# Kernel tuning notes

Measured on AMD Instinct MI355X. Metric: run time of the kernel, lower is better.

## Reference

```python
import jax, jax.numpy as jnp
import numpy as np
from jax import lax

NB = 65536          # voxels (seeds) per batch element
C = 256             # feature dim
NUM_CLASS = 3
MAX_NPOINTS = 4096  # per-batch top-k keep
FPS_NPOINTS = 2048  # farthest-point samples
OFFSET_RANGE = np.array([3.0, 3.0, 2.0], dtype=np.float32)
BN_EPS = 1e-5


def _bn_relu(x, gamma, beta):
    # nn.BatchNorm1d in training mode: batch statistics over N
    m = jnp.mean(x, axis=0)
    v = jnp.var(x, axis=0)
    return jax.nn.relu((x - m) * lax.rsqrt(v + BN_EPS) * gamma + beta)


def _vote_mlp(x, w1, g1, b1, w2, b2):
    # Linear(bias=False) -> BN -> ReLU -> Linear(bias)
    return _bn_relu(x @ w1, g1, b1) @ w2 + b2


def _fps(xyz, k):
    # D-FPS (PointNet++ furthest_point_sample): start at index 0,
    # iteratively pick the point with max min-distance to selected set.
    M = xyz.shape[0]

    def step(carry, _):
        dist, last = carry
        d = jnp.sum((xyz - xyz[last]) ** 2, axis=-1)
        dist = jnp.minimum(dist, d)
        nxt = jnp.argmax(dist).astype(jnp.int32)
        return (dist, nxt), nxt

    init = (jnp.full((M,), 1e10, xyz.dtype), jnp.int32(0))
    _, idxs = lax.scan(step, init, None, length=k - 1)
    return jnp.concatenate([jnp.zeros((1,), jnp.int32), idxs])


def setup_inputs() -> dict:
    key = jax.random.key(0)
    ks = jax.random.split(key, 8)
    B = 4
    N = B * NB
    seed_xyz = jax.random.uniform(ks[0], (N, 3), jnp.float32) * jnp.array([70.0, 80.0, 4.0]) - jnp.array([0.0, 40.0, 3.0])
    seed_feats = jax.random.normal(ks[1], (N, C), jnp.float32)
    s = 0.02
    inp = {
        "seed_xyz": seed_xyz,
        "seed_feats": seed_feats,
        "w_off1": jax.random.normal(ks[2], (C, C), jnp.float32) * s,
        "g_off1": jnp.ones((C,), jnp.float32),
        "be_off1": jnp.zeros((C,), jnp.float32),
        "w_off2": jax.random.normal(ks[3], (C, 3), jnp.float32) * s,
        "b_off2": jnp.zeros((3,), jnp.float32),
        "w_cls1": jax.random.normal(ks[4], (C, C), jnp.float32) * s,
        "g_cls1": jnp.ones((C,), jnp.float32),
        "be_cls1": jnp.zeros((C,), jnp.float32),
        "w_cls2": jax.random.normal(ks[5], (C, NUM_CLASS), jnp.float32) * s,
        "b_cls2": jnp.full((NUM_CLASS,), -2.19, jnp.float32),  # cls bias init fill(-2.19)
        "batch_size": B,
    }
    return inp


def reference(seed_xyz, seed_feats, w_off1, g_off1, be_off1, w_off2, b_off2,
              w_cls1, g_cls1, be_cls1, w_cls2, b_cls2, batch_size):
    B = int(batch_size)
    off_rng = jnp.asarray(OFFSET_RANGE)

    # VoteLayer
    seed_offset = _vote_mlp(seed_feats, w_off1, g_off1, be_off1, w_off2, b_off2)   # (N,3)
    seed_cls = _vote_mlp(seed_feats, w_cls1, g_cls1, be_cls1, w_cls2, b_cls2)      # (N,num_class)
    limited = jnp.clip(seed_offset, -off_rng, off_rng)
    votes_xyz = seed_xyz + limited                                                 # (N,3)

    # fps_pool_layer: per-batch topk + D-FPS
    scores = jnp.max(seed_cls, axis=-1)                                            # (N,)
    scores_b = scores.reshape(B, NB)
    xyz_b = seed_xyz.reshape(B, NB, 3)

    def per_batch(sc, xyz):
        _, topk_idx = lax.top_k(jax.nn.sigmoid(sc), MAX_NPOINTS)   # (K,)
        fidx = _fps(xyz[topk_idx], FPS_NPOINTS)                    # (P,) local in topk set
        return topk_idx[fidx]                                      # remap to per-batch index

    local_idx = jax.vmap(per_batch)(scores_b, xyz_b)               # (B, P)
    fps_indices = (local_idx + jnp.arange(B, dtype=local_idx.dtype)[:, None] * NB).reshape(-1)

    bs_col = jnp.repeat(jnp.arange(B, dtype=jnp.float32), NB)[:, None]
    seeds = jnp.concatenate([bs_col, seed_xyz], axis=-1)           # (N,4)
    votes = jnp.concatenate([bs_col, votes_xyz], axis=-1)          # (N,4)

    vote_candidates = lax.stop_gradient(votes[fps_indices])        # .detach() in torch
    vote_features = seed_feats[fps_indices]                        # (B*P, C)

    return (vote_candidates, vote_features, seeds, seed_cls, votes, fps_indices)
```

## Files before the change

kernel.cpp:

```cpp
#include <hip/hip_runtime.h>

#define NB_V 65536
#define TOPK 4096
#define FPSK 2048

typedef short bf16x8 __attribute__((ext_vector_type(8)));
typedef float f32x4 __attribute__((ext_vector_type(4)));

__global__ __launch_bounds__(256, 2) void k_dualgemm(
    const float* __restrict__ A, const float* __restrict__ Wcls,
    const float* __restrict__ Woff, float* __restrict__ Hcls,
    float* __restrict__ Hoff, double* __restrict__ part_cls,
    float2* __restrict__ part_off, int N) {
  __shared__ __align__(16) char smem[67584];
  const int tid = threadIdx.x;
  const int NCB = (N >> 6) << 1;

  if ((int)blockIdx.x < NCB) {
    float(*Aft)[68] = (float(*)[68])smem;
    float(*Bf)[132] = (float(*)[132])(smem + 8704);
    const int tx = tid & 15, ty = tid >> 4;
    const int cb = blockIdx.x & 1;
    const int rb = blockIdx.x >> 1;
    double acc[4][8];
#pragma unroll
    for (int i = 0; i < 4; ++i)
#pragma unroll
      for (int j = 0; j < 8; ++j) acc[i][j] = 0.0;

    for (int kc = 0; kc < 256; kc += 32) {
#pragma unroll
      for (int l = 0; l < 8; ++l) {
        int f = tid + 256 * l;
        int r = f >> 5, c = f & 31;
        Aft[c][r] = A[(size_t)(rb * 64 + r) * 256 + kc + c];
      }
#pragma unroll
      for (int l = 0; l < 16; ++l) {
        int f = tid + 256 * l;
        int kr = f >> 7, c = f & 127;
        Bf[kr][c] = Wcls[(size_t)(kc + kr) * 256 + cb * 128 + c];
      }
      __syncthreads();
#pragma unroll 4
      for (int kk = 0; kk < 32; ++kk) {
        float4 af = *reinterpret_cast<const float4*>(&Aft[kk][ty * 4]);
        float4 bf0 = *reinterpret_cast<const float4*>(&Bf[kk][tx * 8]);
        float4 bf1 = *reinterpret_cast<const float4*>(&Bf[kk][tx * 8 + 4]);
        double a0[4] = {(double)af.x, (double)af.y, (double)af.z, (double)af.w};
        double b0[8] = {(double)bf0.x, (double)bf0.y, (double)bf0.z, (double)bf0.w,
                        (double)bf1.x, (double)bf1.y, (double)bf1.z, (double)bf1.w};
#pragma unroll
        for (int i = 0; i < 4; ++i)
#pragma unroll
          for (int j = 0; j < 8; ++j) acc[i][j] = fma(a0[i], b0[j], acc[i][j]);
      }
      __syncthreads();
    }
    double s[8], q[8];
#pragma unroll
    for (int j = 0; j < 8; ++j) { s[j] = 0.0; q[j] = 0.0; }
#pragma unroll
    for (int i = 0; i < 4; ++i) {
      float4 h0, h1;
      float hv[8];
#pragma unroll
      for (int j = 0; j < 8; ++j) {
        hv[j] = (float)acc[i][j];
        double d = (double)hv[j];
        s[j] += d;
        q[j] = fma(d, d, q[j]);
      }
      h0 = make_float4(hv[0], hv[1], hv[2], hv[3]);
      h1 = make_float4(hv[4], hv[5], hv[6], hv[7]);
      size_t base = (size_t)(rb * 64 + ty * 4 + i) * 256 + cb * 128 + tx * 8;
      *reinterpret_cast<float4*>(&Hcls[base]) = h0;
      *reinterpret_cast<float4*>(&Hcls[base + 4]) = h1;
    }
    __syncthreads();
    double(*ps)[128] = (double(*)[128])smem;
    double(*pq)[128] = (double(*)[128])(smem + 16384);
#pragma unroll
    for (int j = 0; j < 8; ++j) {
      ps[ty][tx * 8 + j] = s[j];
      pq[ty][tx * 8 + j] = q[j];
    }
    __syncthreads();
    if (tid < 128) {
      double S = 0.0, Q = 0.0;
#pragma unroll
      for (int t = 0; t < 16; ++t) { S += ps[t][tid]; Q += pq[t][tid]; }
      part_cls[(size_t)blockIdx.x * 256 + tid * 2] = S;
      part_cls[(size_t)blockIdx.x * 256 + tid * 2 + 1] = Q;
    }
  } else {
    unsigned short(*As)[264] = (unsigned short(*)[264])smem;
    unsigned short(*Bs)[264] = (unsigned short(*)[264])(smem + 33792);
    const int gb = blockIdx.x - NCB;
    const int cb = gb & 3;
    const int rb = gb >> 2;
#pragma unroll
    for (int l = 0; l < 16; ++l) {
      int f = tid + 256 * l;
      int r = f >> 6, c4 = (f & 63) << 2;
      float4 v = *reinterpret_cast<const float4*>(&A[(size_t)(rb * 64 + r) * 256 + c4]);
      ushort4 u;
      u.x = (unsigned short)(__float_as_uint(v.x) >> 16);
      u.y = (unsigned short)(__float_as_uint(v.y) >> 16);
      u.z = (unsigned short)(__float_as_uint(v.z) >> 16);
      u.w = (unsigned short)(__float_as_uint(v.w) >> 16);
      *reinterpret_cast<ushort4*>(&As[r][c4]) = u;
    }
    {
      const int c = tid & 63;
      const int kg = tid >> 6;
#pragma unroll
      for (int j = 0; j < 16; ++j) {
        int k0 = kg * 64 + j * 4;
        ushort4 u;
        u.x = (unsigned short)(__float_as_uint(Woff[(size_t)(k0 + 0) * 256 + cb * 64 + c]) >> 16);
        u.y = (unsigned short)(__float_as_uint(Woff[(size_t)(k0 + 1) * 256 + cb * 64 + c]) >> 16);
        u.z = (unsigned short)(__float_as_uint(Woff[(size_t)(k0 + 2) * 256 + cb * 64 + c]) >> 16);
        u.w = (unsigned short)(__float_as_uint(Woff[(size_t)(k0 + 3) * 256 + cb * 64 + c]) >> 16);
        *reinterpret_cast<ushort4*>(&Bs[c][k0]) = u;
      }
    }
    __syncthreads();
    const int lane = tid & 63, w = tid >> 6;
    const int m = lane & 15, kq = lane >> 4;
    f32x4 acc[4];
#pragma unroll
    for (int s = 0; s < 4; ++s) acc[s] = (f32x4){0.f, 0.f, 0.f, 0.f};
#pragma unroll
    for (int k0 = 0; k0 < 256; k0 += 32) {
      bf16x8 a = *reinterpret_cast<const bf16x8*>(&As[w * 16 + m][k0 + kq * 8]);
#pragma unroll
      for (int s = 0; s < 4; ++s) {
        bf16x8 bfr = *reinterpret_cast<const bf16x8*>(&Bs[s * 16 + m][k0 + kq * 8]);
        acc[s] = __builtin_amdgcn_mfma_f32_16x16x32_bf16(a, bfr, acc[s], 0, 0, 0);
      }
    }
    double cs[4], cq[4];
#pragma unroll
    for (int s = 0; s < 4; ++s) { cs[s] = 0.0; cq[s] = 0.0; }
#pragma unroll
    for (int s = 0; s < 4; ++s)
#pragma unroll
      for (int i = 0; i < 4; ++i) {
        float hv = acc[s][i];
        Hoff[(size_t)(rb * 64 + w * 16 + kq * 4 + i) * 256 + cb * 64 + s * 16 + m] = hv;
        double d = (double)hv;
        cs[s] += d;
        cq[s] = fma(d, d, cq[s]);
      }
    __syncthreads();
    double(*ps)[64] = (double(*)[64])smem;
    double(*pq)[64] = (double(*)[64])(smem + 8192);
#pragma unroll
    for (int s = 0; s < 4; ++s) {
      ps[w * 4 + kq][s * 16 + m] = cs[s];
      pq[w * 4 + kq][s * 16 + m] = cq[s];
    }
    __syncthreads();
    if (tid < 64) {
      double S = 0.0, Q = 0.0;
#pragma unroll
      for (int t = 0; t < 16; ++t) { S += ps[t][tid]; Q += pq[t][tid]; }
      part_off[(size_t)gb * 64 + tid] = make_float2((float)S, (float)Q);
    }
  }
}

__global__ __launch_bounds__(256) void k_fins(const double* __restrict__ part_cls,
                                              const float2* __restrict__ part_off,
                                              const float* __restrict__ g_cls,
                                              const float* __restrict__ be_cls,
                                              const float* __restrict__ g_off,
                                              const float* __restrict__ be_off,
                                              double* __restrict__ a_cls,
                                              double* __restrict__ c_cls,
                                              double* __restrict__ a_off,
                                              double* __restrict__ c_off, int N) {
  __shared__ double ls[256], lq[256];
  const int tid = threadIdx.x;
  const int nrb = N >> 6;
  double S = 0.0, Q = 0.0;
  if ((int)blockIdx.x < 256) {
    const int c = blockIdx.x;
    const int cbb = c >> 7, cl = c & 127;
    for (int m = 0; m < nrb / 256; ++m) {
      int rb = tid + 256 * m;
      const double* p = part_cls + ((size_t)(rb * 2 + cbb) * 256 + cl * 2);
      S += p[0];
      Q += p[1];
    }
  } else {
    const int c = blockIdx.x - 256;
    const int ccb = c >> 6, cl = c & 63;
    for (int m = 0; m < nrb / 256; ++m) {
      int r2 = tid + 256 * m;
      float2 p = part_off[(size_t)(r2 * 4 + ccb) * 64 + cl];
      S += (double)p.x;
      Q += (double)p.y;
    }
  }
  ls[tid] = S;
  lq[tid] = Q;
  __syncthreads();
  for (int st = 128; st; st >>= 1) {
    if (tid < st) {
      ls[tid] += ls[tid + st];
      lq[tid] += lq[tid + st];
    }
    __syncthreads();
  }
  if (tid == 0) {
    double mean = ls[0] / (double)N;
    double var = lq[0] / (double)N - mean * mean;
    if ((int)blockIdx.x < 256) {
      const int c = blockIdx.x;
      double a = (double)g_cls[c] / sqrt(var + 1e-5);
      a_cls[c] = a;
      c_cls[c] = (double)be_cls[c] - mean * a;
    } else {
      const int c = blockIdx.x - 256;
      double a = (double)g_off[c] / sqrt(var + 1e-5);
      a_off[c] = a;
      c_off[c] = (double)be_off[c] - mean * a;
    }
  }
}

__global__ __launch_bounds__(256) void k_fuse_cls(const float* __restrict__ Hcls,
                                                  const float* __restrict__ xyz,
                                                  const float* __restrict__ w_cls2,
                                                  const float* __restrict__ b_cls2,
                                                  const double* __restrict__ aarr,
                                                  const double* __restrict__ carr,
                                                  float* __restrict__ out_seeds,
                                                  float* __restrict__ out_cls,
                                                  unsigned long long* __restrict__ keys,
                                                  int N) {
  __shared__ double sa[256], sc[256];
  __shared__ double w2[256][3];
  const int tid = threadIdx.x;
  {
    sa[tid] = aarr[tid];
    sc[tid] = carr[tid];
#pragma unroll
    for (int k = 0; k < 3; ++k) w2[tid][k] = (double)w_cls2[tid * 3 + k];
  }
  __syncthreads();
  const int lane = tid & 63, wid = tid >> 6;
  const int gw = blockIdx.x * 4 + wid;
  for (int r = gw; r < N; r += 4096) {
    double pc0 = 0, pc1 = 0, pc2 = 0;
#pragma unroll
    for (int q = 0; q < 4; ++q) {
      int c = lane + 64 * q;
      double h2 = (double)Hcls[(size_t)r * 256 + c];
      double v2 = fma(h2, sa[c], sc[c]);
      v2 = v2 > 0.0 ? v2 : 0.0;
      pc0 = fma(v2, w2[c][0], pc0);
      pc1 = fma(v2, w2[c][1], pc1);
      pc2 = fma(v2, w2[c][2], pc2);
    }
#pragma unroll
    for (int off = 32; off; off >>= 1) {
      pc0 += __shfl_xor(pc0, off);
      pc1 += __shfl_xor(pc1, off);
      pc2 += __shfl_xor(pc2, off);
    }
    if (lane == 0) {
      float x = xyz[(size_t)r * 3], y = xyz[(size_t)r * 3 + 1], z = xyz[(size_t)r * 3 + 2];
      float bs = (float)(r >> 16);
      out_seeds[(size_t)r * 4 + 0] = bs;
      out_seeds[(size_t)r * 4 + 1] = x;
      out_seeds[(size_t)r * 4 + 2] = y;
      out_seeds[(size_t)r * 4 + 3] = z;
      double c0 = pc0 + (double)b_cls2[0];
      double c1 = pc1 + (double)b_cls2[1];
      double c2v = pc2 + (double)b_cls2[2];
      out_cls[(size_t)r * 3 + 0] = (float)c0;
      out_cls[(size_t)r * 3 + 1] = (float)c1;
      out_cls[(size_t)r * 3 + 2] = (float)c2v;
      double s = c0 > c1 ? c0 : c1;
      s = s > c2v ? s : c2v;
      long long bits = __double_as_longlong(s);
      unsigned long long key =
          bits >= 0 ? ((unsigned long long)bits | 0x8000000000000000ull) : ~((unsigned long long)bits);
      keys[r] = key;
    }
  }
}

__global__ __launch_bounds__(1024) void k_topk(const unsigned long long* __restrict__ keys,
                                               unsigned int* __restrict__ topk) {
  const int b = blockIdx.x;
  const unsigned long long* K = keys + (size_t)b * NB_V;
  __shared__ unsigned int hist[256];
  __shared__ unsigned long long pfx_s;
  __shared__ int want_s;
  __shared__ unsigned long long skey[TOPK];
  __shared__ unsigned int sidx[TOPK];
  __shared__ int cnt_hi, cnt_eq;
  __shared__ unsigned int eq_idx[1024];
  const int tid = threadIdx.x;
  const int lane = tid & 63;
  if (tid == 0) { pfx_s = 0ull; want_s = TOPK; }
  __syncthreads();
  for (int p = 0; p < 8; ++p) {
    const int shift = 56 - 8 * p;
    if (tid < 256) hist[tid] = 0;
    __syncthreads();
    unsigned long long pfx = pfx_s;
    for (int i = tid; i < NB_V; i += 1024) {
      unsigned long long k = K[i];
      bool ok;
      if (p == 0) ok = true;
      else ok = ((k >> (shift + 8)) == (pfx >> (shift + 8)));
      unsigned bin = ok ? (unsigned)((k >> shift) & 255u) : 0xFFFFFFFFu;
      unsigned long long okm = __ballot(ok);
      if (okm) {
        int leader = __ffsll((unsigned long long)okm) - 1;
        unsigned pb = __shfl(bin, leader);
        unsigned long long m = __ballot(ok && bin == pb);
        if (lane == leader) atomicAdd(&hist[pb], (unsigned)__popcll(m));
        if (ok && bin != pb) atomicAdd(&hist[bin], 1u);
      }
    }
    __syncthreads();
    if (tid == 0) {
      int want = want_s;
      int cum = 0, d = 255;
      for (; d >= 0; --d) {
        int c = (int)hist[d];
        if (cum + c >= want) break;
        cum += c;
      }
      want_s = want - cum;
      pfx_s = pfx_s | ((unsigned long long)d << shift);
    }
    __syncthreads();
  }
  const unsigned long long Kthr = pfx_s;
  const int T = want_s;
  if (tid == 0) { cnt_hi = 0; cnt_eq = 0; }
  __syncthreads();
  for (int i = tid; i < NB_V; i += 1024) {
    unsigned long long k = K[i];
    if (k > Kthr) {
      int pos = atomicAdd(&cnt_hi, 1);
      skey[pos] = k;
      sidx[pos] = (unsigned)i;
    } else if (k == Kthr) {
      int pos = atomicAdd(&cnt_eq, 1);
      if (pos < 1024) eq_idx[pos] = (unsigned)i;
    }
  }
  __syncthreads();
  if (tid == 0) {
    int m = cnt_eq; if (m > 1024) m = 1024;
    for (int a2 = 1; a2 < m; ++a2) {
      unsigned v = eq_idx[a2];
      int b2 = a2 - 1;
      while (b2 >= 0 && eq_idx[b2] > v) { eq_idx[b2 + 1] = eq_idx[b2]; --b2; }
      eq_idx[b2 + 1] = v;
    }
    for (int t = 0; t < T; ++t) { skey[cnt_hi + t] = Kthr; sidx[cnt_hi + t] = eq_idx[t]; }
  }
  __syncthreads();
  for (int k2 = 2; k2 <= TOPK; k2 <<= 1) {
    for (int j = k2 >> 1; j > 0; j >>= 1) {
      for (int i = tid; i < TOPK; i += 1024) {
        int ix = i ^ j;
        if (ix > i) {
          unsigned long long ka = skey[i], kb = skey[ix];
          unsigned int ia = sidx[i], ib = sidx[ix];
          bool a_first = (ka > kb) || (ka == kb && ia < ib);
          bool up = (i & k2) == 0;
          if (up ? !a_first : a_first) {
            skey[i] = kb; skey[ix] = ka;
            sidx[i] = ib; sidx[ix] = ia;
          }
        }
      }
      __syncthreads();
    }
  }
  for (int i = tid; i < TOPK; i += 1024) topk[(size_t)b * TOPK + i] = sidx[i];
}

template <int CTRL>
__device__ __forceinline__ void dpp_merge2(unsigned long long& v, int& p) {
  unsigned lo = (unsigned)v, hi = (unsigned)(v >> 32);
  unsigned olo = (unsigned)__builtin_amdgcn_update_dpp(0, (int)lo, CTRL, 0xF, 0xF, false);
  unsigned ohi = (unsigned)__builtin_amdgcn_update_dpp(0, (int)hi, CTRL, 0xF, 0xF, false);
  int op = __builtin_amdgcn_update_dpp(0, p, CTRL, 0xF, 0xF, false);
  unsigned long long ov = ((unsigned long long)ohi << 32) | (unsigned long long)olo;
  bool t = (ov > v) || (ov == v && op < p);
  v = t ? ov : v;
  p = t ? op : p;
}

__device__ __forceinline__ void shfl_merge2(unsigned long long& v, int& p, int mask) {
  unsigned long long ov = __shfl_xor(v, mask);
  int op = __shfl_xor(p, mask);
  bool t = (ov > v) || (ov == v && op < p);
  v = t ? ov : v;
  p = t ? op : p;
}

#define FPS_REP16(M) M(0) M(1) M(2) M(3) M(4) M(5) M(6) M(7) \
                     M(8) M(9) M(10) M(11) M(12) M(13) M(14) M(15)

__global__ __launch_bounds__(256, 1) void k_fused2(const float* __restrict__ xyz,
                                                   const unsigned int* __restrict__ topk,
                                                   unsigned int* __restrict__ fpspos,
                                                   const float* __restrict__ Hoff,
                                                   const double* __restrict__ a_off,
                                                   const double* __restrict__ c_off,
                                                   const float* __restrict__ w_off2,
                                                   const float* __restrict__ b_off2,
                                                   float* __restrict__ out_votes, int N) {
  __shared__ __align__(16) char smem[82944];
  const int tid = threadIdx.x;

  if (blockIdx.x < 4) {
    float4* cpos = (float4*)smem;
    ulonglong2(*wv)[4] = (ulonglong2(*)[4])(smem + 65536);
    float4(*wc)[4] = (float4(*)[4])(smem + 65792);
    const int b = blockIdx.x;

#define FPS_DECL(J) float x##J, y##J, z##J; double d##J;
    FPS_REP16(FPS_DECL)

#define FPS_INIT(J) { \
    int p = tid + 256 * (J); \
    unsigned idx = topk[(size_t)b * TOPK + p]; \
    size_t base = ((size_t)b * NB_V + idx) * 3; \
    x##J = xyz[base]; y##J = xyz[base + 1]; z##J = xyz[base + 2]; \
    d##J = 1e10; \
    cpos[p] = make_float4(x##J, y##J, z##J, 0.0f); }
    FPS_REP16(FPS_INIT)

    if (tid == 0) {
      wc[0][0] = make_float4(x0, y0, z0, 0.0f);
      fpspos[(size_t)b * FPSK] = 0u;
    }
    __syncthreads();
    float4 s0 = wc[0][0];
    float sx = s0.x, sy = s0.y, sz = s0.z;
    const int lane = tid & 63, wid = tid >> 6;

    for (int it = 1; it < FPSK; ++it) {
      const int par = it & 1;
      double lx = (double)sx, ly = (double)sy, lz = (double)sz;
      unsigned long long cv0, cv1;
      int cp0, cp1;
#define FPS_UPD(J) { \
    double dx = (double)x##J - lx; \
    double dy = (double)y##J - ly; \
    double dz = (double)z##J - lz; \
    double dd = __dadd_rn(__dadd_rn(__dmul_rn(dx, dx), __dmul_rn(dy, dy)), __dmul_rn(dz, dz)); \
    d##J = fmin(d##J, dd); \
    unsigned long long db = (unsigned long long)__double_as_longlong(d##J); \
    if ((J) == 0) { cv0 = db; cp0 = tid; } \
    else if ((J) == 1) { cv1 = db; cp1 = tid + 256; } \
    else if (((J) & 1) == 0) { bool g = db > cv0; cv0 = g ? db : cv0; cp0 = g ? (tid + 256 * (J)) : cp0; } \
    else { bool g = db > cv1; cv1 = g ? db : cv1; cp1 = g ? (tid + 256 * (J)) : cp1; } }
      FPS_REP16(FPS_UPD)
      {
        bool g = (cv1 > cv0) || (cv1 == cv0 && cp1 < cp0);
        cv0 = g ? cv1 : cv0;
        cp0 = g ? cp1 : cp0;
      }
      dpp_merge2<0xB1>(cv0, cp0);
      dpp_merge2<0x4E>(cv0, cp0);
      dpp_merge2<0x124>(cv0, cp0);
      dpp_merge2<0x128>(cv0, cp0);
      shfl_merge2(cv0, cp0, 16);
      shfl_merge2(cv0, cp0, 32);
      float4 wpos = cpos[cp0];
      if (lane == 0) {
        wv[par][wid] = make_ulonglong2(cv0, (unsigned long long)(unsigned)cp0);
        wc[par][wid] = wpos;
      }
      __syncthreads();
      ulonglong2 e0 = wv[par][0];
      float4 q0 = wc[par][0];
      unsigned long long bv = e0.x;
      int bp = (int)e0.y;
      float fx = q0.x, fy = q0.y, fz = q0.z;
#pragma unroll
      for (int w = 1; w < 4; ++w) {
        ulonglong2 e = wv[par][w];
        float4 q = wc[par][w];
        bool t = (e.x > bv) || (e.x == bv && (int)e.y < bp);
        bv = t ? e.x : bv;
        bp = t ? (int)e.y : bp;
        fx = t ? q.x : fx;
        fy = t ? q.y : fy;
        fz = t ? q.z : fz;
      }
      sx = fx; sy = fy; sz = fz;
      if (tid == 0) fpspos[(size_t)b * FPSK + it] = (unsigned)bp;
    }
  } else {
    const int fb = blockIdx.x - 4;
    double* sa = (double*)smem;
    double* sc = (double*)(smem + 2048);
    double(*w2)[3] = (double(*)[3])(smem + 4096);
    {
      sa[tid] = a_off[tid];
      sc[tid] = c_off[tid];
#pragma unroll
      for (int k = 0; k < 3; ++k) w2[tid][k] = (double)w_off2[tid * 3 + k];
    }
    __syncthreads();
    const int lane = tid & 63, wid = tid >> 6;
    const int gw = fb * 4 + wid;
    for (int r = gw; r < N; r += 4096) {
      double po0 = 0, po1 = 0, po2 = 0;
#pragma unroll
      for (int q = 0; q < 4; ++q) {
        int c = lane + 64 * q;
        double h = (double)Hoff[(size_t)r * 256 + c];
        double v = fma(h, sa[c], sc[c]);
        v = v > 0.0 ? v : 0.0;
        po0 = fma(v, w2[c][0], po0);
        po1 = fma(v, w2[c][1], po1);
        po2 = fma(v, w2[c][2], po2);
      }
#pragma unroll
      for (int off = 32; off; off >>= 1) {
        po0 += __shfl_xor(po0, off);
        po1 += __shfl_xor(po1, off);
        po2 += __shfl_xor(po2, off);
      }
      if (lane == 0) {
        float x = xyz[(size_t)r * 3], y = xyz[(size_t)r * 3 + 1], z = xyz[(size_t)r * 3 + 2];
        float bs = (float)(r >> 16);
        double offv[3] = {po0 + (double)b_off2[0], po1 + (double)b_off2[1], po2 + (double)b_off2[2]};
        const double rng[3] = {3.0, 3.0, 2.0};
        float pxyz[3] = {x, y, z};
        out_votes[(size_t)r * 4 + 0] = bs;
#pragma unroll
        for (int k = 0; k < 3; ++k) {
          double lim = offv[k];
          lim = lim < -rng[k] ? -rng[k] : lim;
          lim = lim > rng[k] ? rng[k] : lim;
          out_votes[(size_t)r * 4 + 1 + k] = (float)((double)pxyz[k] + lim);
        }
      }
    }
  }
}

__global__ __launch_bounds__(256) void k_gather(const unsigned int* __restrict__ topk,
                                                const unsigned int* __restrict__ fpspos,
                                                const float* __restrict__ feats,
                                                const float* __restrict__ votes_out,
                                                float* __restrict__ o0, float* __restrict__ o1,
                                                float* __restrict__ o5) {
  const int r = blockIdx.x;
  const int b = r / FPSK;
  __shared__ unsigned int gsh;
  if (threadIdx.x == 0) {
    unsigned pos = fpspos[r];
    unsigned local = topk[(size_t)b * TOPK + pos];
    gsh = (unsigned)(b * NB_V) + local;
  }
  __syncthreads();
  const unsigned g = gsh;
  o1[(size_t)r * 256 + threadIdx.x] = feats[(size_t)g * 256 + threadIdx.x];
  if (threadIdx.x < 4) o0[(size_t)r * 4 + threadIdx.x] = votes_out[(size_t)g * 4 + threadIdx.x];
  if (threadIdx.x == 4) o5[r] = (float)g;
}

extern "C" void kernel_launch(void* const* d_in, const int* in_sizes, int n_in,
                              void* d_out, int out_size, void* d_ws, size_t ws_size,
                              hipStream_t stream) {
  const float* xyz = (const float*)d_in[0];
  const float* feats = (const float*)d_in[1];
  const float* w_off1 = (const float*)d_in[2];
  const float* g_off1 = (const float*)d_in[3];
  const float* be_off1 = (const float*)d_in[4];
  const float* w_off2 = (const float*)d_in[5];
  const float* b_off2 = (const float*)d_in[6];
  const float* w_cls1 = (const float*)d_in[7];
  const float* g_cls1 = (const float*)d_in[8];
  const float* be_cls1 = (const float*)d_in[9];
  const float* w_cls2 = (const float*)d_in[10];
  const float* b_cls2 = (const float*)d_in[11];

  const int N = in_sizes[0] / 3;
  const int B = N / NB_V;
  const int BP = B * FPSK;

  float* out = (float*)d_out;
  float* o0 = out;
  float* o1 = o0 + (size_t)BP * 4;
  float* o2 = o1 + (size_t)BP * 256;
  float* o3 = o2 + (size_t)N * 4;
  float* o4 = o3 + (size_t)N * 3;
  float* o5 = o4 + (size_t)N * 4;

  char* w = (char*)d_ws;
  float* Hoff = (float*)w;
  float* Hcls = (float*)(w + (size_t)N * 1024);
  char* p0 = w + (size_t)N * 2048;
  double* part_cls = (double*)p0;
  float2* part_off = (float2*)(p0 + 16777216);
  char* p1 = p0 + 16777216 + 8388608;
  double* a_cls = (double*)p1;
  double* c_cls = a_cls + 256;
  double* a_off = c_cls + 256;
  double* c_off = a_off + 256;
  unsigned long long* keys = (unsigned long long*)(p1 + 8192);
  unsigned int* topkbuf = (unsigned int*)((char*)keys + (size_t)N * 8);
  unsigned int* fpspos = topkbuf + (size_t)B * TOPK;

  const int NCB = (N / 64) * 2;
  const int NGB = (N / 64) * 4;
  k_dualgemm<<<dim3(NCB + NGB), dim3(256), 0, stream>>>(feats, w_cls1, w_off1, Hcls, Hoff,
                                                        part_cls, part_off, N);
  k_fins<<<dim3(512), dim3(256), 0, stream>>>(part_cls, part_off, g_cls1, be_cls1,
                                              g_off1, be_off1, a_cls, c_cls, a_off, c_off, N);
  k_fuse_cls<<<dim3(1024), dim3(256), 0, stream>>>(Hcls, xyz, w_cls2, b_cls2, a_cls, c_cls,
                                                   o2, o3, keys, N);
  k_topk<<<dim3(B), dim3(1024), 0, stream>>>(keys, topkbuf);
  k_fused2<<<dim3(4 + 1024), dim3(256), 0, stream>>>(xyz, topkbuf, fpspos, Hoff, a_off,
                                                     c_off, w_off2, b_off2, o4, N);
  k_gather<<<dim3(BP), dim3(256), 0, stream>>>(topkbuf, fpspos, feats, o4, o0, o1, o5);
}
```

Baseline: 3.499 ms.

## Store GEMM tiles as doubles in LDS and widen FPS blocks to 512 threads

The cls GEMM path now converts A and W to double when loading them into shared memory. It uses a padded B layout and a strided row mapping, which removes the per-iteration float-to-double conversions in the inner loop, at the cost of more LDS traffic. The FPS/offset kernel moves to 512-thread blocks, so each thread holds 8 points instead of 16 and the cross-wave reduction spans 8 waves. This aims to shorten each serial FPS iteration but adds barrier and reduction overhead. The offset-path blocks are halved in count to keep total work coverage the same.

After: 4.156 ms. 1.19x slower.

```diff
diff --git a/kernel.cpp b/kernel.cpp
--- a/kernel.cpp
+++ b/kernel.cpp
@@ -17,8 +17,8 @@
   const int NCB = (N >> 6) << 1;
 
   if ((int)blockIdx.x < NCB) {
-    float(*Aft)[68] = (float(*)[68])smem;
-    float(*Bf)[132] = (float(*)[132])(smem + 8704);
+    double(*Asm)[33] = (double(*)[33])smem;
+    double* BfF = (double*)(smem + 16896);
     const int tx = tid & 15, ty = tid >> 4;
     const int cb = blockIdx.x & 1;
     const int rb = blockIdx.x >> 1;
@@ -33,23 +33,27 @@
       for (int l = 0; l < 8; ++l) {
         int f = tid + 256 * l;
         int r = f >> 5, c = f & 31;
-        Aft[c][r] = A[(size_t)(rb * 64 + r) * 256 + kc + c];
+        Asm[r][c] = (double)A[(size_t)(rb * 64 + r) * 256 + kc + c];
       }
 #pragma unroll
       for (int l = 0; l < 16; ++l) {
         int f = tid + 256 * l;
         int kr = f >> 7, c = f & 127;
-        Bf[kr][c] = Wcls[(size_t)(kc + kr) * 256 + cb * 128 + c];
+        BfF[kr * 160 + (c >> 3) * 10 + (c & 7)] =
+            (double)Wcls[(size_t)(kc + kr) * 256 + cb * 128 + c];
       }
       __syncthreads();
 #pragma unroll 4
       for (int kk = 0; kk < 32; ++kk) {
-        float4 af = *reinterpret_cast<const float4*>(&Aft[kk][ty * 4]);
-        float4 bf0 = *reinterpret_cast<const float4*>(&Bf[kk][tx * 8]);
-        float4 bf1 = *reinterpret_cast<const float4*>(&Bf[kk][tx * 8 + 4]);
-        double a0[4] = {(double)af.x, (double)af.y, (double)af.z, (double)af.w};
-        double b0[8] = {(double)bf0.x, (double)bf0.y, (double)bf0.z, (double)bf0.w,
-                        (double)bf1.x, (double)bf1.y, (double)bf1.z, (double)bf1.w};
+        double a0[4];
+#pragma unroll
+        for (int i = 0; i < 4; ++i) a0[i] = Asm[ty + 16 * i][kk];
+        const double* bR = BfF + kk * 160 + tx * 10;
+        double2 b01 = *reinterpret_cast<const double2*>(bR);
+        double2 b23 = *reinterpret_cast<const double2*>(bR + 2);
+        double2 b45 = *reinterpret_cast<const double2*>(bR + 4);
+        double2 b67 = *reinterpret_cast<const double2*>(bR + 6);
+        double b0[8] = {b01.x, b01.y, b23.x, b23.y, b45.x, b45.y, b67.x, b67.y};
 #pragma unroll
         for (int i = 0; i < 4; ++i)
 #pragma unroll
@@ -62,7 +66,6 @@
     for (int j = 0; j < 8; ++j) { s[j] = 0.0; q[j] = 0.0; }
 #pragma unroll
     for (int i = 0; i < 4; ++i) {
-      float4 h0, h1;
       float hv[8];
 #pragma unroll
       for (int j = 0; j < 8; ++j) {
@@ -71,11 +74,9 @@
         s[j] += d;
         q[j] = fma(d, d, q[j]);
       }
-      h0 = make_float4(hv[0], hv[1], hv[2], hv[3]);
-      h1 = make_float4(hv[4], hv[5], hv[6], hv[7]);
-      size_t base = (size_t)(rb * 64 + ty * 4 + i) * 256 + cb * 128 + tx * 8;
-      *reinterpret_cast<float4*>(&Hcls[base]) = h0;
-      *reinterpret_cast<float4*>(&Hcls[base + 4]) = h1;
+      size_t base = (size_t)(rb * 64 + ty + 16 * i) * 256 + cb * 128 + tx * 8;
+      *reinterpret_cast<float4*>(&Hcls[base]) = make_float4(hv[0], hv[1], hv[2], hv[3]);
+      *reinterpret_cast<float4*>(&Hcls[base + 4]) = make_float4(hv[4], hv[5], hv[6], hv[7]);
     }
     __syncthreads();
     double(*ps)[128] = (double(*)[128])smem;
@@ -411,10 +412,9 @@
   p = t ? op : p;
 }
 
-#define FPS_REP16(M) M(0) M(1) M(2) M(3) M(4) M(5) M(6) M(7) \
-                     M(8) M(9) M(10) M(11) M(12) M(13) M(14) M(15)
-
-__global__ __launch_bounds__(256, 1) void k_fused2(const float* __restrict__ xyz,
+#define FPS_REP8(M) M(0) M(1) M(2) M(3) M(4) M(5) M(6) M(7)
+
+__global__ __launch_bounds__(512, 1) void k_fused2(const float* __restrict__ xyz,
                                                    const unsigned int* __restrict__ topk,
                                                    unsigned int* __restrict__ fpspos,
                                                    const float* __restrict__ Hoff,
@@ -428,21 +428,21 @@
 
   if (blockIdx.x < 4) {
     float4* cpos = (float4*)smem;
-    ulonglong2(*wv)[4] = (ulonglong2(*)[4])(smem + 65536);
-    float4(*wc)[4] = (float4(*)[4])(smem + 65792);
+    ulonglong2(*wv)[8] = (ulonglong2(*)[8])(smem + 65536);
+    float4(*wc)[8] = (float4(*)[8])(smem + 65536 + 256);
     const int b = blockIdx.x;
 
 #define FPS_DECL(J) float x##J, y##J, z##J; double d##J;
-    FPS_REP16(FPS_DECL)
+    FPS_REP8(FPS_DECL)
 
 #define FPS_INIT(J) { \
-    int p = tid + 256 * (J); \
+    int p = tid + 512 * (J); \
     unsigned idx = topk[(size_t)b * TOPK + p]; \
     size_t base = ((size_t)b * NB_V + idx) * 3; \
     x##J = xyz[base]; y##J = xyz[base + 1]; z##J = xyz[base + 2]; \
     d##J = 1e10; \
     cpos[p] = make_float4(x##J, y##J, z##J, 0.0f); }
-    FPS_REP16(FPS_INIT)
+    FPS_REP8(FPS_INIT)
 
     if (tid == 0) {
       wc[0][0] = make_float4(x0, y0, z0, 0.0f);
@@ -466,10 +466,10 @@
     d##J = fmin(d##J, dd); \
     unsigned long long db = (unsigned long long)__double_as_longlong(d##J); \
     if ((J) == 0) { cv0 = db; cp0 = tid; } \
-    else if ((J) == 1) { cv1 = db; cp1 = tid + 256; } \
-    else if (((J) & 1) == 0) { bool g = db > cv0; cv0 = g ? db : cv0; cp0 = g ? (tid + 256 * (J)) : cp0; } \
-    else { bool g = db > cv1; cv1 = g ? db : cv1; cp1 = g ? (tid + 256 * (J)) : cp1; } }
-      FPS_REP16(FPS_UPD)
+    else if ((J) == 1) { cv1 = db; cp1 = tid + 512; } \
+    else if (((J) & 1) == 0) { bool g = db > cv0; cv0 = g ? db : cv0; cp0 = g ? (tid + 512 * (J)) : cp0; } \
+    else { bool g = db > cv1; cv1 = g ? db : cv1; cp1 = g ? (tid + 512 * (J)) : cp1; } }
+      FPS_REP8(FPS_UPD)
       {
         bool g = (cv1 > cv0) || (cv1 == cv0 && cp1 < cp0);
         cv0 = g ? cv1 : cv0;
@@ -493,7 +493,7 @@
       int bp = (int)e0.y;
       float fx = q0.x, fy = q0.y, fz = q0.z;
 #pragma unroll
-      for (int w = 1; w < 4; ++w) {
+      for (int w = 1; w < 8; ++w) {
         ulonglong2 e = wv[par][w];
         float4 q = wc[par][w];
         bool t = (e.x > bv) || (e.x == bv && (int)e.y < bp);
@@ -511,7 +511,7 @@
     double* sa = (double*)smem;
     double* sc = (double*)(smem + 2048);
     double(*w2)[3] = (double(*)[3])(smem + 4096);
-    {
+    if (tid < 256) {
       sa[tid] = a_off[tid];
       sc[tid] = c_off[tid];
 #pragma unroll
@@ -519,7 +519,7 @@
     }
     __syncthreads();
     const int lane = tid & 63, wid = tid >> 6;
-    const int gw = fb * 4 + wid;
+    const int gw = fb * 8 + wid;
     for (int r = gw; r < N; r += 4096) {
       double po0 = 0, po1 = 0, po2 = 0;
 #pragma unroll
@@ -630,7 +630,7 @@
   k_fuse_cls<<<dim3(1024), dim3(256), 0, stream>>>(Hcls, xyz, w_cls2, b_cls2, a_cls, c_cls,
                                                    o2, o3, keys, N);
   k_topk<<<dim3(B), dim3(1024), 0, stream>>>(keys, topkbuf);
-  k_fused2<<<dim3(4 + 1024), dim3(256), 0, stream>>>(xyz, topkbuf, fpspos, Hoff, a_off,
-                                                     c_off, w_off2, b_off2, o4, N);
+  k_fused2<<<dim3(4 + 512), dim3(512), 0, stream>>>(xyz, topkbuf, fpspos, Hoff, a_off,
+                                                    c_off, w_off2, b_off2, o4, N);
   k_gather<<<dim3(BP), dim3(256), 0, stream>>>(topkbuf, fpspos, feats, o4, o0, o1, o5);
 }
```
